# Kernel optimization log

Hardware: AMD Instinct MI355X
Metric: run time of the kernel (lower is better)

The kernel has to match this reference:

```python
import jax, jax.numpy as jnp
import numpy as np

ALPHA = 0.1
K = 10


def setup_inputs() -> dict:
    key = jax.random.key(0)
    k1, k2, k3, k4, k5, k6 = jax.random.split(key, 6)
    N, F_in, H = 100000, 256, 128
    E, E_lp = 1600000, 400000
    return {
        "x": jax.random.normal(k1, (N, F_in), dtype=jnp.float32),
        "edge_index": jax.random.randint(k2, (2, E), 0, N, dtype=jnp.int64),
        "pos_edge_index": jax.random.randint(k3, (2, E_lp), 0, N, dtype=jnp.int64),
        "neg_edge_index": jax.random.randint(k4, (2, E_lp), 0, N, dtype=jnp.int64),
        "W1": jax.random.normal(k5, (F_in, H), dtype=jnp.float32) * (1.0 / np.sqrt(F_in)),
        "W2": jax.random.normal(k6, (H, H), dtype=jnp.float32) * (1.0 / np.sqrt(H)),
    }


def _appnp_propagate(h, src, dst, norm, num_nodes):
    # z_{k+1} = (1-alpha) * A_hat z_k + alpha * h   (K hops)
    z = h
    for _ in range(K):
        msg = norm[:, None] * z[src]                         # [E+N, d] gather
        agg = jax.ops.segment_sum(msg, dst, num_segments=num_nodes)  # scatter-add
        z = (1.0 - ALPHA) * agg + ALPHA * h
    return z


def reference(x, edge_index, pos_edge_index, neg_edge_index, W1, W2):
    N = x.shape[0]
    # add self-loops, GCN symmetric normalization: d^-1/2 A_sl d^-1/2
    loops = jnp.arange(N, dtype=edge_index.dtype)
    src = jnp.concatenate([edge_index[0], loops])
    dst = jnp.concatenate([edge_index[1], loops])
    deg = jax.ops.segment_sum(jnp.ones_like(dst, dtype=x.dtype), dst, num_segments=N)
    dinv = jax.lax.rsqrt(jnp.maximum(deg, 1.0))
    norm = dinv[src] * dinv[dst]

    # encode: two APPNP layers with ReLU in between (drop_rate = 0)
    z = _appnp_propagate(x @ W1, src, dst, norm, N)
    z = jax.nn.relu(z)
    z = _appnp_propagate(z @ W2, src, dst, norm, N)

    # decode: edge dot products over concatenated pos/neg edges
    e = jnp.concatenate([pos_edge_index, neg_edge_index], axis=-1)
    return jnp.sum(z[e[0]] * z[e[1]], axis=-1)
```

## Files before the change

### kernel.cpp

```cpp
#include <hip/hip_runtime.h>


constexpr int Hd = 128;
constexpr int Fin = 256;
constexpr float A_ = 0.1f;
constexpr float OMA = 0.9f;

typedef float vf2 __attribute__((ext_vector_type(2)));
typedef __bf16 bf16x8 __attribute__((ext_vector_type(8)));
typedef float f32x4 __attribute__((ext_vector_type(4)));

__device__ __forceinline__ int idx_at(const void* p, size_t i, int is64) {
    if (is64) return (int)((const long long*)p)[i];
    return ((const int*)p)[i];
}

__device__ __forceinline__ unsigned short bf16_of(float x) {
    unsigned u = __float_as_uint(x);
    return (unsigned short)((u + 0x7fffu + ((u >> 16) & 1u)) >> 16);
}

__device__ __forceinline__ unsigned pack_bf16x2(float x, float y) {
    unsigned ux = __float_as_uint(x);
    unsigned uy = __float_as_uint(y);
    ux = (ux + 0x7fffu + ((ux >> 16) & 1u)) >> 16;
    uy = (uy + 0x7fffu + ((uy >> 16) & 1u)) & 0xffff0000u;
    return ux | uy;
}

__device__ __forceinline__ float2 unpack_bf16x2(unsigned v) {
    float2 r;
    r.x = __uint_as_float(v << 16);
    r.y = __uint_as_float(v & 0xffff0000u);
    return r;
}

__device__ __forceinline__ unsigned short pack_fp8x2(float x, float y) {
    int v = __builtin_amdgcn_cvt_pk_fp8_f32(x, y, 0, false);
    return (unsigned short)(unsigned)v;
}

__device__ __forceinline__ float2 unpack_fp8x2(unsigned short v) {
    vf2 r = __builtin_amdgcn_cvt_pk_f32_fp8((int)(unsigned)v, false);
    float2 o;
    o.x = r[0];
    o.y = r[1];
    return o;
}

__global__ void k_detect(const int* __restrict__ p, int npairs, int* __restrict__ flag) {
    __shared__ int any32;
    if (threadIdx.x == 0) any32 = 0;
    __syncthreads();
    for (int i = threadIdx.x; i < npairs; i += blockDim.x)
        if (p[2 * i + 1] != 0) any32 = 1;
    __syncthreads();
    if (threadIdx.x == 0) *flag = any32 ? 0 : 1;
}


__global__ void k_zero_i32(int* __restrict__ p, int n) {
    int i = blockIdx.x * blockDim.x + threadIdx.x;
    if (i < n) p[i] = 0;
}

__global__ void k_count(const void* __restrict__ ei, int E, int* __restrict__ cnt,
                        const int* __restrict__ flag) {
    int is64 = *flag;
    int e = blockIdx.x * blockDim.x + threadIdx.x;
    if (e < E) {
        int d = idx_at(ei, (size_t)E + e, is64);
        atomicAdd(&cnt[d], 1);
    }
}

__global__ void k_dinv(const int* __restrict__ cnt, float* __restrict__ dinv, int N) {
    int i = blockIdx.x * blockDim.x + threadIdx.x;
    if (i < N) dinv[i] = rsqrtf((float)(cnt[i] + 1));
}

__global__ void k_scan1(const int* __restrict__ cnt, int* __restrict__ rp,
                        int* __restrict__ bsum, int N) {
    __shared__ int s[256];
    int t = threadIdx.x;
    int i = blockIdx.x * 256 + t;
    int v = (i < N) ? (cnt[i] + 1) : 0;
    s[t] = v;
    __syncthreads();
    for (int off = 1; off < 256; off <<= 1) {
        int add = (t >= off) ? s[t - off] : 0;
        __syncthreads();
        s[t] += add;
        __syncthreads();
    }
    if (i < N) rp[i] = s[t] - v;
    if (t == 255) bsum[blockIdx.x] = s[255];
}

__global__ void k_scan2(int* __restrict__ bsum, int nb) {
    __shared__ int s[512];
    int t = threadIdx.x;
    int v = (t < nb) ? bsum[t] : 0;
    s[t] = v;
    __syncthreads();
    for (int off = 1; off < 512; off <<= 1) {
        int add = (t >= off) ? s[t - off] : 0;
        __syncthreads();
        s[t] += add;
        __syncthreads();
    }
    if (t < nb) bsum[t] = s[t] - v;
}

__global__ void k_scan3(int* __restrict__ rp, const int* __restrict__ bsum,
                        int* __restrict__ cursor, const float* __restrict__ dinv,
                        int2* __restrict__ cw, int N, int Etot) {
    int i = blockIdx.x * blockDim.x + threadIdx.x;
    if (i < N) {
        int r = rp[i] + bsum[i >> 8];
        rp[i] = r;
        cursor[i] = 1;
        float d = dinv[i];
        int2 p;
        p.x = i;
        p.y = __float_as_int(OMA * d * d);
        cw[r] = p;
    }
    if (i == 0) rp[N] = Etot;
}

__global__ __launch_bounds__(256) void k_place(const void* __restrict__ ei, int E,
                                               const int* __restrict__ rp,
                                               int* __restrict__ cursor,
                                               const float* __restrict__ dinv,
                                               int2* __restrict__ cw,
                                               const int* __restrict__ flag) {
    const int is64 = *flag;
    const int e0 = (blockIdx.x * blockDim.x + threadIdx.x) * 4;
    if (e0 >= E) return;
    const int n = min(4, E - e0);
    int s[4], d[4];
#pragma unroll
    for (int k = 0; k < 4; ++k) {
        int e = e0 + min(k, n - 1);
        s[k] = idx_at(ei, (size_t)e, is64);
        d[k] = idx_at(ei, (size_t)E + e, is64);
    }
    int pos[4];
#pragma unroll
    for (int k = 0; k < 4; ++k)
        if (k < n) pos[k] = rp[d[k]] + atomicAdd(&cursor[d[k]], 1);
    float ws[4], wd[4];
#pragma unroll
    for (int k = 0; k < 4; ++k) {
        ws[k] = dinv[s[k]];
        wd[k] = dinv[d[k]];
    }
#pragma unroll
    for (int k = 0; k < 4; ++k)
        if (k < n) {
            int2 p;
            p.x = s[k];
            p.y = __float_as_int(OMA * ws[k] * wd[k]);
            cw[pos[k]] = p;
        }
}

__global__ void k_wt(const float* __restrict__ W, unsigned short* __restrict__ Wt, int K) {
    int i = blockIdx.x * blockDim.x + threadIdx.x;
    if (i < K * 128) {
        int k = i >> 7, c = i & 127;
        Wt[c * K + k] = bf16_of(W[i]);
    }
}


template <int KTOT, bool AF32>
__global__ __launch_bounds__(256) void k_gemm_mfma(const void* __restrict__ Ap,
                                                   const unsigned short* __restrict__ Wt,
                                                   unsigned short* __restrict__ z0,
                                                   unsigned* __restrict__ ah, int N) {
    __shared__ __align__(16) char smem[64 * 132 * 4];
    unsigned short (*As)[40] = (unsigned short(*)[40])smem;
    unsigned short (*Bs)[40] = (unsigned short(*)[40])(smem + 5120);
    float (*Cs)[132] = (float(*)[132])smem;

    const int t    = threadIdx.x;
    const int lane = t & 63;
    const int w    = t >> 6;
    const int wr   = w >> 1;
    const int wc   = w & 1;
    const int r0   = blockIdx.x * 64;

    f32x4 acc[2][4];
#pragma unroll
    for (int i = 0; i < 2; ++i)
#pragma unroll
        for (int j = 0; j < 4; ++j)
#pragma unroll
            for (int q = 0; q < 4; ++q) acc[i][j][q] = 0.f;

    const int arow = t >> 2;
    const int akc  = (t & 3) * 8;
    const int bcol = t >> 1;
    const int bkc  = (t & 1) * 16;

    for (int k0 = 0; k0 < KTOT; k0 += 32) {
        {
            int gr = r0 + arow;
            if (AF32) {
                uint4 s = make_uint4(0, 0, 0, 0);
                if (gr < N) {
                    const float* a = (const float*)Ap + (size_t)gr * KTOT + k0 + akc;
                    float4 v0 = *(const float4*)a;
                    float4 v1 = *(const float4*)(a + 4);
                    s.x = pack_bf16x2(v0.x, v0.y);
                    s.y = pack_bf16x2(v0.z, v0.w);
                    s.z = pack_bf16x2(v1.x, v1.y);
                    s.w = pack_bf16x2(v1.z, v1.w);
                }
                *(uint4*)&As[arow][akc] = s;
            } else {
                uint4 s = make_uint4(0, 0, 0, 0);
                if (gr < N) s = *(const uint4*)((const unsigned short*)Ap + (size_t)gr * KTOT + k0 + akc);
                *(uint4*)&As[arow][akc] = s;
            }
        }
        {
            const unsigned short* wsrc = Wt + (size_t)bcol * KTOT + k0 + bkc;
            *(uint4*)&Bs[bcol][bkc]     = *(const uint4*)wsrc;
            *(uint4*)&Bs[bcol][bkc + 8] = *(const uint4*)(wsrc + 8);
        }
        __syncthreads();
        {
            const int kblk = (lane >> 4) * 8;
            const int l15  = lane & 15;
            bf16x8 af[2], bfr[4];
#pragma unroll
            for (int i = 0; i < 2; ++i)
                af[i] = *(const bf16x8*)&As[wr * 32 + i * 16 + l15][kblk];
#pragma unroll
            for (int j = 0; j < 4; ++j)
                bfr[j] = *(const bf16x8*)&Bs[wc * 64 + j * 16 + l15][kblk];
#pragma unroll
            for (int i = 0; i < 2; ++i)
#pragma unroll
                for (int j = 0; j < 4; ++j)
                    acc[i][j] = __builtin_amdgcn_mfma_f32_16x16x32_bf16(af[i], bfr[j], acc[i][j], 0, 0, 0);
        }
        __syncthreads();
    }

    {
        const int l15 = lane & 15;
        const int rq  = (lane >> 4) * 4;
#pragma unroll
        for (int i = 0; i < 2; ++i)
#pragma unroll
            for (int j = 0; j < 4; ++j)
#pragma unroll
                for (int q = 0; q < 4; ++q)
                    Cs[wr * 32 + i * 16 + rq + q][wc * 64 + j * 16 + l15] = acc[i][j][q];
    }
    __syncthreads();
    {
        const int row = t >> 2;
        const int cb  = (t & 3) * 32;
        const int gr  = r0 + row;
        if (gr < N) {
            float c[32];
#pragma unroll
            for (int m = 0; m < 8; ++m) {
                float4 v = *(const float4*)&Cs[row][cb + m * 4];
                c[m * 4 + 0] = v.x; c[m * 4 + 1] = v.y; c[m * 4 + 2] = v.z; c[m * 4 + 3] = v.w;
            }
            unsigned pk[8];
#pragma unroll
            for (int m = 0; m < 8; ++m) {
                unsigned lo = (unsigned)pack_fp8x2(c[4 * m + 0], c[4 * m + 1]);
                unsigned hi = (unsigned)pack_fp8x2(c[4 * m + 2], c[4 * m + 3]);
                pk[m] = lo | (hi << 16);
            }
            uint4* zd = (uint4*)&z0[((size_t)gr << 6) + (cb >> 1)];
            zd[0] = make_uint4(pk[0], pk[1], pk[2], pk[3]);
            zd[1] = make_uint4(pk[4], pk[5], pk[6], pk[7]);
            unsigned am[16];
#pragma unroll
            for (int m = 0; m < 16; ++m)
                am[m] = pack_bf16x2(A_ * c[2 * m], A_ * c[2 * m + 1]);
            uint4* ad = (uint4*)&ah[((size_t)gr << 6) + (cb >> 1)];
            ad[0] = make_uint4(am[0],  am[1],  am[2],  am[3]);
            ad[1] = make_uint4(am[4],  am[5],  am[6],  am[7]);
            ad[2] = make_uint4(am[8],  am[9],  am[10], am[11]);
            ad[3] = make_uint4(am[12], am[13], am[14], am[15]);
        }
    }
}


template <int B, int IN8>
__device__ __forceinline__ void hop_batch(const void* __restrict__ zb,
                                          const int2* __restrict__ cw,
                                          int e, int lane,
                                          float& ax, float& ay,
                                          float& bx, float& by) {
    int2 p[B];
#pragma unroll
    for (int k = 0; k < B; ++k) p[k] = cw[e + k];
    unsigned zv[B];
#pragma unroll
    for (int k = 0; k < B; ++k) {
        if (IN8) zv[k] = ((const unsigned short*)zb)[((unsigned)p[k].x << 6) + lane];
        else     zv[k] = ((const unsigned*)zb)[((unsigned)p[k].x << 6) + lane];
    }
#pragma unroll
    for (int k = 0; k < B; ++k) {
        float wv = __int_as_float(p[k].y);
        float2 z = IN8 ? unpack_fp8x2((unsigned short)zv[k]) : unpack_bf16x2(zv[k]);
        if (k & 1) { bx = fmaf(wv, z.x, bx); by = fmaf(wv, z.y, by); }
        else       { ax = fmaf(wv, z.x, ax); ay = fmaf(wv, z.y, ay); }
    }
}

template <int IN8, int OUTM>
__global__ __launch_bounds__(256) void k_hop(const void* __restrict__ zin,
                                             const unsigned* __restrict__ ah,
                                             void* __restrict__ zout,
                                             const int* __restrict__ rp,
                                             const int2* __restrict__ cw, int N) {
    int wid  = (blockIdx.x * blockDim.x + threadIdx.x) >> 6;
    int lane = threadIdx.x & 63;
    if (wid >= N) return;

    int e   = __builtin_amdgcn_readfirstlane(rp[wid]);
    int end = __builtin_amdgcn_readfirstlane(rp[wid + 1]);

    float2 hh = unpack_bf16x2(ah[((size_t)wid << 6) + lane]);

    float ax = 0.f, ay = 0.f, bx = 0.f, by = 0.f;

    for (; e + 16 <= end; e += 16)
        hop_batch<16, IN8>(zin, cw, e, lane, ax, ay, bx, by);
    if (e + 8 <= end) { hop_batch<8, IN8>(zin, cw, e, lane, ax, ay, bx, by); e += 8; }
    if (e + 4 <= end) { hop_batch<4, IN8>(zin, cw, e, lane, ax, ay, bx, by); e += 4; }
    for (; e < end; ++e) {
        int2 p = cw[e];
        unsigned zv;
        if (IN8) zv = ((const unsigned short*)zin)[((unsigned)p.x << 6) + lane];
        else     zv = ((const unsigned*)zin)[((unsigned)p.x << 6) + lane];
        float2 z = IN8 ? unpack_fp8x2((unsigned short)zv) : unpack_bf16x2(zv);
        float wv = __int_as_float(p.y);
        ax = fmaf(wv, z.x, ax); ay = fmaf(wv, z.y, ay);
    }

    float ox = (ax + bx) + hh.x;
    float oy = (ay + by) + hh.y;
    if (OUTM == 0) {
        ((unsigned short*)zout)[((size_t)wid << 6) + lane] = pack_fp8x2(ox, oy);
    } else if (OUTM == 1) {
        ((unsigned*)zout)[((size_t)wid << 6) + lane] = pack_bf16x2(ox, oy);
    } else {
        ((unsigned*)zout)[((size_t)wid << 6) + lane] =
            pack_bf16x2(fmaxf(ox, 0.f), fmaxf(oy, 0.f));
    }
}


__global__ __launch_bounds__(256) void k_decode(const unsigned* __restrict__ z,
                                                const void* __restrict__ pos,
                                                const void* __restrict__ neg,
                                                float* __restrict__ out, int P, int Q,
                                                const int* __restrict__ flag) {
    int is64 = *flag;
    int t   = blockIdx.x * blockDim.x + threadIdx.x;
    int j   = t >> 4;
    int sub = t & 15;
    if (j >= P + Q) return;
    int a, b;
    if (j < P) { a = idx_at(pos, (size_t)j, is64); b = idx_at(pos, (size_t)P + j, is64); }
    else       { int jj = j - P; a = idx_at(neg, (size_t)jj, is64); b = idx_at(neg, (size_t)Q + jj, is64); }
    const uint4* za = (const uint4*)&z[(size_t)a << 6];
    const uint4* zb = (const uint4*)&z[(size_t)b << 6];
    uint4 va = za[sub];
    uint4 vb = zb[sub];
    float s = 0.f;
    {
        float2 xa, xb;
        xa = unpack_bf16x2(va.x); xb = unpack_bf16x2(vb.x);
        s += xa.x * xb.x + xa.y * xb.y;
        xa = unpack_bf16x2(va.y); xb = unpack_bf16x2(vb.y);
        s += xa.x * xb.x + xa.y * xb.y;
        xa = unpack_bf16x2(va.z); xb = unpack_bf16x2(vb.z);
        s += xa.x * xb.x + xa.y * xb.y;
        xa = unpack_bf16x2(va.w); xb = unpack_bf16x2(vb.w);
        s += xa.x * xb.x + xa.y * xb.y;
    }
#pragma unroll
    for (int off = 8; off >= 1; off >>= 1) s += __shfl_xor(s, off, 16);
    if (sub == 0) out[j] = s;
}


extern "C" void kernel_launch(void* const* d_in, const int* in_sizes, int n_in,
                              void* d_out, int out_size, void* d_ws, size_t ws_size,
                              hipStream_t stream) {
    const float* x   = (const float*)d_in[0];
    const void*  ei  = d_in[1];
    const void*  pos = d_in[2];
    const void*  neg = d_in[3];
    const float* W1  = (const float*)d_in[4];
    const float* W2  = (const float*)d_in[5];
    float*       out = (float*)d_out;

    const int N = in_sizes[0] / Fin;
    const int E = in_sizes[1] / 2;
    const int P = in_sizes[2] / 2;
    const int Q = in_sizes[3] / 2;
    const int Etot = E + N;

    char*  ws  = (char*)d_ws;
    size_t off = 0;
    auto carve = [&](size_t bytes) -> void* {
        void* p = ws + off;
        off = (off + bytes + 511) & ~(size_t)511;
        return p;
    };
    unsigned short* f0   = (unsigned short*)carve((size_t)N * 64 * 2);
    unsigned short* f1   = (unsigned short*)carve((size_t)N * 64 * 2);
    unsigned*       zB2  = (unsigned*)carve((size_t)N * 64 * 4);
    unsigned*       zRB  = (unsigned*)carve((size_t)N * 64 * 4);
    unsigned*       ah   = (unsigned*)carve((size_t)N * 64 * 4);
    unsigned short* Wt1  = (unsigned short*)carve((size_t)128 * 256 * 2);
    unsigned short* Wt2  = (unsigned short*)carve((size_t)128 * 128 * 2);
    float*          dinv = (float*)carve((size_t)N * 4);
    int*     cnt    = (int*)carve((size_t)N * 4);
    int*     rp     = (int*)carve((size_t)(N + 1) * 4);
    int*     cursor = (int*)carve((size_t)N * 4);
    int2*    cw     = (int2*)carve((size_t)Etot * 8);
    int      nb     = (N + 255) / 256;
    int*     bsum   = (int*)carve((size_t)nb * 4);
    int*     flag   = (int*)carve(4);
    (void)ws_size;

    const int gN = (N + 255) / 256;
    const int gE = (E + 255) / 256;

    k_detect<<<1, 256, 0, stream>>>((const int*)ei, 4096, flag);
    k_zero_i32<<<gN, 256, 0, stream>>>(cnt, N);
    k_count<<<gE, 256, 0, stream>>>(ei, E, cnt, flag);
    k_dinv<<<gN, 256, 0, stream>>>(cnt, dinv, N);
    k_scan1<<<nb, 256, 0, stream>>>(cnt, rp, bsum, N);
    k_scan2<<<1, 512, 0, stream>>>(bsum, nb);
    k_scan3<<<gN, 256, 0, stream>>>(rp, bsum, cursor, dinv, cw, N, Etot);
    k_place<<<(E + 1023) / 1024, 256, 0, stream>>>(ei, E, rp, cursor, dinv, cw, flag);
    k_wt<<<(256 * 128 + 255) / 256, 256, 0, stream>>>(W1, Wt1, Fin);
    k_wt<<<(128 * 128 + 255) / 256, 256, 0, stream>>>(W2, Wt2, Hd);

    const int gGemm = (N + 63) / 64;
    const int gHop  = (N * 64 + 255) / 256;

    unsigned short* fb[2] = {f0, f1};

    k_gemm_mfma<Fin, true><<<gGemm, 256, 0, stream>>>(x, Wt1, f0, ah, N);
    for (int k = 0; k < 9; ++k)
        k_hop<1, 0><<<gHop, 256, 0, stream>>>(fb[k & 1], ah, fb[(k + 1) & 1], rp, cw, N);
    k_hop<1, 3><<<gHop, 256, 0, stream>>>(f1, ah, zRB, rp, cw, N);

    k_gemm_mfma<Hd, false><<<gGemm, 256, 0, stream>>>(zRB, Wt2, f0, ah, N);
    for (int k = 0; k < 9; ++k)
        k_hop<1, 0><<<gHop, 256, 0, stream>>>(fb[k & 1], ah, fb[(k + 1) & 1], rp, cw, N);
    k_hop<1, 1><<<gHop, 256, 0, stream>>>(f1, ah, zB2, rp, cw, N);

    const int gDec = ((P + Q) * 16 + 255) / 256;
    k_decode<<<gDec, 256, 0, stream>>>(zB2, pos, neg, out, P, Q, flag);
}
```

Measured before the change: 1.052 ms.

## Factor symmetric normalization out of edges, store prescaled features and int CSR

Rewrites the propagation as D^-1/2 A D^-1/2 by storing features prescaled by dinv, so each edge needs only a column index rather than a (col, weight) pair. The CSR edge array halves from 8 to 4 bytes per edge, and the per-edge FMA becomes a plain add, with the dinv scaling applied once per destination node. The GEMM epilogue and the hop output prescale by dinv before FP8 packing. This changes the FP8 quantization range, which could affect accuracy.

```diff
diff --git a/kernel.cpp b/kernel.cpp
--- a/kernel.cpp
+++ b/kernel.cpp
@@ -113,18 +113,14 @@
 }
 
 __global__ void k_scan3(int* __restrict__ rp, const int* __restrict__ bsum,
-                        int* __restrict__ cursor, const float* __restrict__ dinv,
-                        int2* __restrict__ cw, int N, int Etot) {
+                        int* __restrict__ cursor, int* __restrict__ col,
+                        int N, int Etot) {
     int i = blockIdx.x * blockDim.x + threadIdx.x;
     if (i < N) {
         int r = rp[i] + bsum[i >> 8];
         rp[i] = r;
         cursor[i] = 1;
-        float d = dinv[i];
-        int2 p;
-        p.x = i;
-        p.y = __float_as_int(OMA * d * d);
-        cw[r] = p;
+        col[r] = i;
     }
     if (i == 0) rp[N] = Etot;
 }
@@ -132,8 +128,7 @@
 __global__ __launch_bounds__(256) void k_place(const void* __restrict__ ei, int E,
                                                const int* __restrict__ rp,
                                                int* __restrict__ cursor,
-                                               const float* __restrict__ dinv,
-                                               int2* __restrict__ cw,
+                                               int* __restrict__ col,
                                                const int* __restrict__ flag) {
     const int is64 = *flag;
     const int e0 = (blockIdx.x * blockDim.x + threadIdx.x) * 4;
@@ -150,20 +145,9 @@
 #pragma unroll
     for (int k = 0; k < 4; ++k)
         if (k < n) pos[k] = rp[d[k]] + atomicAdd(&cursor[d[k]], 1);
-    float ws[4], wd[4];
-#pragma unroll
-    for (int k = 0; k < 4; ++k) {
-        ws[k] = dinv[s[k]];
-        wd[k] = dinv[d[k]];
-    }
 #pragma unroll
     for (int k = 0; k < 4; ++k)
-        if (k < n) {
-            int2 p;
-            p.x = s[k];
-            p.y = __float_as_int(OMA * ws[k] * wd[k]);
-            cw[pos[k]] = p;
-        }
+        if (k < n) col[pos[k]] = s[k];
 }
 
 __global__ void k_wt(const float* __restrict__ W, unsigned short* __restrict__ Wt, int K) {
@@ -178,6 +162,7 @@
 template <int KTOT, bool AF32>
 __global__ __launch_bounds__(256) void k_gemm_mfma(const void* __restrict__ Ap,
                                                    const unsigned short* __restrict__ Wt,
+                                                   const float* __restrict__ dinv,
                                                    unsigned short* __restrict__ z0,
                                                    unsigned* __restrict__ ah, int N) {
     __shared__ __align__(16) char smem[64 * 132 * 4];
@@ -268,6 +253,7 @@
         const int cb  = (t & 3) * 32;
         const int gr  = r0 + row;
         if (gr < N) {
+            float dv = dinv[gr];
             float c[32];
 #pragma unroll
             for (int m = 0; m < 8; ++m) {
@@ -277,8 +263,8 @@
             unsigned pk[8];
 #pragma unroll
             for (int m = 0; m < 8; ++m) {
-                unsigned lo = (unsigned)pack_fp8x2(c[4 * m + 0], c[4 * m + 1]);
-                unsigned hi = (unsigned)pack_fp8x2(c[4 * m + 2], c[4 * m + 3]);
+                unsigned lo = (unsigned)pack_fp8x2(dv * c[4 * m + 0], dv * c[4 * m + 1]);
+                unsigned hi = (unsigned)pack_fp8x2(dv * c[4 * m + 2], dv * c[4 * m + 3]);
                 pk[m] = lo | (hi << 16);
             }
             uint4* zd = (uint4*)&z0[((size_t)gr << 6) + (cb >> 1)];
@@ -298,65 +284,59 @@
 }
 
 
-template <int B, int IN8>
-__device__ __forceinline__ void hop_batch(const void* __restrict__ zb,
-                                          const int2* __restrict__ cw,
+template <int B>
+__device__ __forceinline__ void hop_batch(const unsigned short* __restrict__ yb,
+                                          const int* __restrict__ col,
                                           int e, int lane,
                                           float& ax, float& ay,
                                           float& bx, float& by) {
-    int2 p[B];
-#pragma unroll
-    for (int k = 0; k < B; ++k) p[k] = cw[e + k];
-    unsigned zv[B];
+    int c[B];
+#pragma unroll
+    for (int k = 0; k < B; ++k) c[k] = col[e + k];
+    unsigned short v[B];
+#pragma unroll
+    for (int k = 0; k < B; ++k) v[k] = yb[((unsigned)c[k] << 6) + lane];
 #pragma unroll
     for (int k = 0; k < B; ++k) {
-        if (IN8) zv[k] = ((const unsigned short*)zb)[((unsigned)p[k].x << 6) + lane];
-        else     zv[k] = ((const unsigned*)zb)[((unsigned)p[k].x << 6) + lane];
-    }
-#pragma unroll
-    for (int k = 0; k < B; ++k) {
-        float wv = __int_as_float(p[k].y);
-        float2 z = IN8 ? unpack_fp8x2((unsigned short)zv[k]) : unpack_bf16x2(zv[k]);
-        if (k & 1) { bx = fmaf(wv, z.x, bx); by = fmaf(wv, z.y, by); }
-        else       { ax = fmaf(wv, z.x, ax); ay = fmaf(wv, z.y, ay); }
-    }
-}
-
-template <int IN8, int OUTM>
-__global__ __launch_bounds__(256) void k_hop(const void* __restrict__ zin,
+        float2 z = unpack_fp8x2(v[k]);
+        if (k & 1) { bx += z.x; by += z.y; }
+        else       { ax += z.x; ay += z.y; }
+    }
+}
+
+template <int OUTM>
+__global__ __launch_bounds__(256) void k_hop(const unsigned short* __restrict__ yin,
                                              const unsigned* __restrict__ ah,
+                                             const float* __restrict__ dinv,
                                              void* __restrict__ zout,
                                              const int* __restrict__ rp,
-                                             const int2* __restrict__ cw, int N) {
+                                             const int* __restrict__ col, int N) {
     int wid  = (blockIdx.x * blockDim.x + threadIdx.x) >> 6;
     int lane = threadIdx.x & 63;
     if (wid >= N) return;
 
     int e   = __builtin_amdgcn_readfirstlane(rp[wid]);
     int end = __builtin_amdgcn_readfirstlane(rp[wid + 1]);
+    float dv = dinv[wid];
 
     float2 hh = unpack_bf16x2(ah[((size_t)wid << 6) + lane]);
 
     float ax = 0.f, ay = 0.f, bx = 0.f, by = 0.f;
 
     for (; e + 16 <= end; e += 16)
-        hop_batch<16, IN8>(zin, cw, e, lane, ax, ay, bx, by);
-    if (e + 8 <= end) { hop_batch<8, IN8>(zin, cw, e, lane, ax, ay, bx, by); e += 8; }
-    if (e + 4 <= end) { hop_batch<4, IN8>(zin, cw, e, lane, ax, ay, bx, by); e += 4; }
+        hop_batch<16>(yin, col, e, lane, ax, ay, bx, by);
+    if (e + 8 <= end) { hop_batch<8>(yin, col, e, lane, ax, ay, bx, by); e += 8; }
+    if (e + 4 <= end) { hop_batch<4>(yin, col, e, lane, ax, ay, bx, by); e += 4; }
     for (; e < end; ++e) {
-        int2 p = cw[e];
-        unsigned zv;
-        if (IN8) zv = ((const unsigned short*)zin)[((unsigned)p.x << 6) + lane];
-        else     zv = ((const unsigned*)zin)[((unsigned)p.x << 6) + lane];
-        float2 z = IN8 ? unpack_fp8x2((unsigned short)zv) : unpack_bf16x2(zv);
-        float wv = __int_as_float(p.y);
-        ax = fmaf(wv, z.x, ax); ay = fmaf(wv, z.y, ay);
-    }
-
-    float ox = (ax + bx) + hh.x;
-    float oy = (ay + by) + hh.y;
+        float2 z = unpack_fp8x2(yin[((unsigned)col[e] << 6) + lane]);
+        ax += z.x; ay += z.y;
+    }
+
+    float q  = OMA * dv;
+    float ox = q * (ax + bx) + hh.x;
+    float oy = q * (ay + by) + hh.y;
     if (OUTM == 0) {
-        ((unsigned short*)zout)[((size_t)wid << 6) + lane] = pack_fp8x2(ox, oy);
+        ((unsigned short*)zout)[((size_t)wid << 6) + lane] = pack_fp8x2(dv * ox, dv * oy);
     } else if (OUTM == 1) {
         ((unsigned*)zout)[((size_t)wid << 6) + lane] = pack_bf16x2(ox, oy);
     } else {
@@ -436,7 +416,7 @@
     int*     cnt    = (int*)carve((size_t)N * 4);
     int*     rp     = (int*)carve((size_t)(N + 1) * 4);
     int*     cursor = (int*)carve((size_t)N * 4);
-    int2*    cw     = (int2*)carve((size_t)Etot * 8);
+    int*     col    = (int*)carve((size_t)Etot * 4);
     int      nb     = (N + 255) / 256;
     int*     bsum   = (int*)carve((size_t)nb * 4);
     int*     flag   = (int*)carve(4);
@@ -451,8 +431,8 @@
     k_dinv<<<gN, 256, 0, stream>>>(cnt, dinv, N);
     k_scan1<<<nb, 256, 0, stream>>>(cnt, rp, bsum, N);
     k_scan2<<<1, 512, 0, stream>>>(bsum, nb);
-    k_scan3<<<gN, 256, 0, stream>>>(rp, bsum, cursor, dinv, cw, N, Etot);
-    k_place<<<(E + 1023) / 1024, 256, 0, stream>>>(ei, E, rp, cursor, dinv, cw, flag);
+    k_scan3<<<gN, 256, 0, stream>>>(rp, bsum, cursor, col, N, Etot);
+    k_place<<<(E + 1023) / 1024, 256, 0, stream>>>(ei, E, rp, cursor, col, flag);
     k_wt<<<(256 * 128 + 255) / 256, 256, 0, stream>>>(W1, Wt1, Fin);
     k_wt<<<(128 * 128 + 255) / 256, 256, 0, stream>>>(W2, Wt2, Hd);
 
@@ -461,15 +441,15 @@
 
     unsigned short* fb[2] = {f0, f1};
 
-    k_gemm_mfma<Fin, true><<<gGemm, 256, 0, stream>>>(x, Wt1, f0, ah, N);
+    k_gemm_mfma<Fin, true><<<gGemm, 256, 0, stream>>>(x, Wt1, dinv, f0, ah, N);
     for (int k = 0; k < 9; ++k)
-        k_hop<1, 0><<<gHop, 256, 0, stream>>>(fb[k & 1], ah, fb[(k + 1) & 1], rp, cw, N);
-    k_hop<1, 3><<<gHop, 256, 0, stream>>>(f1, ah, zRB, rp, cw, N);
-
-    k_gemm_mfma<Hd, false><<<gGemm, 256, 0, stream>>>(zRB, Wt2, f0, ah, N);
+        k_hop<0><<<gHop, 256, 0, stream>>>(fb[k & 1], ah, dinv, fb[(k + 1) & 1], rp, col, N);
+    k_hop<3><<<gHop, 256, 0, stream>>>(f1, ah, dinv, zRB, rp, col, N);
+
+    k_gemm_mfma<Hd, false><<<gGemm, 256, 0, stream>>>(zRB, Wt2, dinv, f0, ah, N);
     for (int k = 0; k < 9; ++k)
-        k_hop<1, 0><<<gHop, 256, 0, stream>>>(fb[k & 1], ah, fb[(k + 1) & 1], rp, cw, N);
-    k_hop<1, 1><<<gHop, 256, 0, stream>>>(f1, ah, zB2, rp, cw, N);
+        k_hop<0><<<gHop, 256, 0, stream>>>(fb[k & 1], ah, dinv, fb[(k + 1) & 1], rp, col, N);
+    k_hop<1><<<gHop, 256, 0, stream>>>(f1, ah, dinv, zB2, rp, col, N);
 
     const int gDec = ((P + Q) * 16 + 255) / 256;
     k_decode<<<gDec, 256, 0, stream>>>(zB2, pos, neg, out, P, Q, flag);
```

After: 1.042 ms. No clear change (-0.9%).
